# Performance work log

Measured on AMD Instinct MI355X. Metric: run time of the kernel, lower is better.

## Reference

```python
import jax, jax.numpy as jnp
import numpy as np

N_NODES = 100000
N_EDGES = 1600000
IN_CH, HID_CH, OUT_CH = 128, 128, 40


def setup_inputs() -> dict:
    key = jax.random.key(0)
    ks = jax.random.split(key, 7)
    s = 1.0 / np.sqrt(IN_CH)
    s2 = 1.0 / np.sqrt(HID_CH)
    return {
        "x": jax.random.normal(ks[0], (N_NODES, IN_CH), jnp.float32),
        "edge_index": jax.random.randint(ks[1], (2, N_EDGES), 0, N_NODES, jnp.int64),
        "W1l": jax.random.normal(ks[2], (IN_CH, HID_CH), jnp.float32) * s,
        "b1": jnp.zeros((HID_CH,), jnp.float32),
        "W1r": jax.random.normal(ks[3], (IN_CH, HID_CH), jnp.float32) * s,
        "W2l": jax.random.normal(ks[4], (HID_CH, OUT_CH), jnp.float32) * s2,
        "b2": jnp.zeros((OUT_CH,), jnp.float32),
        "W2r": jax.random.normal(ks[5], (HID_CH, OUT_CH), jnp.float32) * s2,
    }


def reference(x, edge_index, W1l, b1, W1r, W2l, b2, W2r):
    src, dst = edge_index[0], edge_index[1]
    # per-target in-degree for mean aggregation (zero-degree nodes -> 0 output)
    deg = jax.ops.segment_sum(jnp.ones((src.shape[0],), x.dtype), dst,
                              num_segments=N_NODES)
    inv_deg = jnp.where(deg > 0, 1.0 / jnp.maximum(deg, 1.0), 0.0)[:, None]

    def sage(h, Wl, b, Wr):
        # gather source features, scatter-sum to targets, normalize -> mean
        agg = jax.ops.segment_sum(h[src], dst, num_segments=N_NODES) * inv_deg
        return agg @ Wl + b + h @ Wr

    h = jax.nn.relu(sage(x, W1l, b1, W1r))
    # F.dropout(p=0.5) defaults to training=True -> active dropout
    keep = jax.random.bernoulli(jax.random.key(42), 0.5, h.shape)
    h = jnp.where(keep, h * 2.0, 0.0)
    out = sage(h, W2l, b2, W2r)
    return jax.nn.log_softmax(out, axis=1)
```

## Files before the change

kernel.cpp:

```cpp
#include <hip/hip_runtime.h>
#include <stdint.h>
#include <stddef.h>

#define N_NODES 100000
#define N_EDGES 1600000
#define IN_CH 128
#define HID_CH 128
#define OUT_CH 40

#define NB 196
#define GCAP 10240
#define TILE_EDGES 2048
#define LCAP 40

#define N_MASK_WORDS 400000
#define N_CVT4 3200000

typedef __attribute__((ext_vector_type(8))) short bf16x8;
typedef __attribute__((ext_vector_type(8))) unsigned short u16x8;
typedef __attribute__((ext_vector_type(4))) float f32x4;

__device__ __forceinline__ ushort f2bf(float f) {
    uint32_t u = __float_as_uint(f);
    uint32_t r = (u + 0x7FFFu + ((u >> 16) & 1u)) >> 16;
    return (ushort)r;
}
__device__ __forceinline__ float bf2f(ushort u) {
    return __uint_as_float(((uint32_t)u) << 16);
}

__device__ __forceinline__ uint32_t rotl32(uint32_t x, int r) {
    return (x << r) | (x >> (32 - r));
}

__device__ __forceinline__ void threefry2x32_k42(uint32_t x0, uint32_t x1,
                                                 uint32_t& o0, uint32_t& o1) {
    const uint32_t ks0 = 0u, ks1 = 42u;
    const uint32_t ks2 = 0u ^ 42u ^ 0x1BD11BDAu;
    x0 += ks0; x1 += ks1;
    x0 += x1; x1 = rotl32(x1, 13); x1 ^= x0;
    x0 += x1; x1 = rotl32(x1, 15); x1 ^= x0;
    x0 += x1; x1 = rotl32(x1, 26); x1 ^= x0;
    x0 += x1; x1 = rotl32(x1,  6); x1 ^= x0;
    x0 += ks1; x1 += ks2 + 1u;
    x0 += x1; x1 = rotl32(x1, 17); x1 ^= x0;
    x0 += x1; x1 = rotl32(x1, 29); x1 ^= x0;
    x0 += x1; x1 = rotl32(x1, 16); x1 ^= x0;
    x0 += x1; x1 = rotl32(x1, 24); x1 ^= x0;
    x0 += ks2; x1 += ks0 + 2u;
    x0 += x1; x1 = rotl32(x1, 13); x1 ^= x0;
    x0 += x1; x1 = rotl32(x1, 15); x1 ^= x0;
    x0 += x1; x1 = rotl32(x1, 26); x1 ^= x0;
    x0 += x1; x1 = rotl32(x1,  6); x1 ^= x0;
    x0 += ks0; x1 += ks1 + 3u;
    x0 += x1; x1 = rotl32(x1, 17); x1 ^= x0;
    x0 += x1; x1 = rotl32(x1, 29); x1 ^= x0;
    x0 += x1; x1 = rotl32(x1, 16); x1 ^= x0;
    x0 += x1; x1 = rotl32(x1, 24); x1 ^= x0;
    x0 += ks1; x1 += ks2 + 4u;
    x0 += x1; x1 = rotl32(x1, 13); x1 ^= x0;
    x0 += x1; x1 = rotl32(x1, 15); x1 ^= x0;
    x0 += x1; x1 = rotl32(x1, 26); x1 ^= x0;
    x0 += x1; x1 = rotl32(x1,  6); x1 ^= x0;
    x0 += ks2; x1 += ks0 + 5u;
    o0 = x0; o1 = x1;
}

__device__ __forceinline__ void load_edge(const void* ei, bool is32, int e,
                                          int& s, int& d) {
    if (is32) {
        const int* p = (const int*)ei;
        s = p[e]; d = p[N_EDGES + e];
    } else {
        const long long* p = (const long long*)ei;
        s = (int)p[e]; d = (int)p[N_EDGES + e];
    }
}

__global__ __launch_bounds__(256) void prep(const int* __restrict__ ei32,
                                            int* __restrict__ flag,
                                            int* __restrict__ gcnt) {
    const int t = threadIdx.x;
    if (blockIdx.x == 0) {
        __shared__ int red[256];
        int local = 0;
        #pragma unroll
        for (int j = 0; j < 64; ++j) {
            int k = (t * 64 + j) * 97;
            local |= ei32[2 * k + 1];
        }
        red[t] = local;
        __syncthreads();
        for (int off = 128; off; off >>= 1) {
            if (t < off) red[t] |= red[t + off];
            __syncthreads();
        }
        if (t == 0) *flag = (red[0] != 0);
    } else {
        for (int i = t; i < NB * 16; i += 256) gcnt[i] = 0;
    }
}

__global__ __launch_bounds__(256) void bucket_edges(
    const void* __restrict__ ei, const int* __restrict__ flag,
    int* __restrict__ gcnt, uint2* __restrict__ gbuf) {
    __shared__ uint2 lbuf[NB][LCAP];
    __shared__ int lcnt[NB];
    const bool is32 = (*flag != 0);
    const int t = threadIdx.x;
    for (int b = t; b < NB; b += 256) lcnt[b] = 0;
    __syncthreads();
    const int base = blockIdx.x * TILE_EDGES;
    #pragma unroll
    for (int j = 0; j < TILE_EDGES / 256; ++j) {
        int e = base + j * 256 + t;
        if (e < N_EDGES) {
            int s, d;
            load_edge(ei, is32, e, s, d);
            int b = d >> 9;
            int pos = atomicAdd(&lcnt[b], 1);
            if (pos < LCAP) {
                lbuf[b][pos] = make_uint2((uint32_t)s, (uint32_t)d);
            } else {
                int gp = atomicAdd(&gcnt[b * 16], 1);
                gbuf[(size_t)b * GCAP + gp] = make_uint2((uint32_t)s, (uint32_t)d);
            }
        }
    }
    __syncthreads();
    if (t < NB) {
        int cnt = lcnt[t];
        if (cnt > LCAP) cnt = LCAP;
        if (cnt > 0) {
            int gp = atomicAdd(&gcnt[t * 16], cnt);
            uint2* dst = gbuf + (size_t)t * GCAP + gp;
            for (int i = 0; i < cnt; ++i) dst[i] = lbuf[t][i];
        }
    }
}

__global__ void bucket_scan(const int* __restrict__ gcnt, int* __restrict__ bbase) {
    __shared__ int s[256];
    int t = threadIdx.x;
    int tot = (t < NB) ? gcnt[t * 16] : 0;
    s[t] = tot;
    __syncthreads();
    for (int off = 1; off < 256; off <<= 1) {
        int a = (t >= off) ? s[t - off] : 0;
        __syncthreads();
        s[t] += a;
        __syncthreads();
    }
    if (t < NB) bbase[t] = s[t] - tot;
}

__global__ __launch_bounds__(256) void build_csr(
    const int* __restrict__ gcnt, const uint2* __restrict__ gbuf,
    const int* __restrict__ bbase, int* __restrict__ csr, int* __restrict__ cursor) {
    __shared__ int hist[512];
    __shared__ int excl[512];
    __shared__ int cur[512];
    __shared__ int psum[256];
    const int b = blockIdx.x;
    const int t = threadIdx.x;
    hist[t] = 0; hist[t + 256] = 0;
    __syncthreads();
    const int base = bbase[b];
    const int cnt = gcnt[b * 16];
    const uint2* src = gbuf + (size_t)b * GCAP;
    for (int i = t; i < cnt; i += 256)
        atomicAdd(&hist[src[i].y & 511], 1);
    __syncthreads();
    int h0 = hist[2 * t], h1 = hist[2 * t + 1];
    psum[t] = h0 + h1;
    __syncthreads();
    int v = psum[t];
    for (int off = 1; off < 256; off <<= 1) {
        int a = (t >= off) ? psum[t - off] : 0;
        __syncthreads();
        psum[t] += a;
        __syncthreads();
    }
    int pex = psum[t] - v;
    excl[2 * t] = pex;
    excl[2 * t + 1] = pex + h0;
    cur[2 * t] = pex;
    cur[2 * t + 1] = pex + h0;
    __syncthreads();
    for (int j = t; j < 512; j += 256) {
        int node = b * 512 + j;
        if (node < N_NODES) cursor[node] = base + excl[j] + hist[j];
    }
    for (int i = t; i < cnt; i += 256) {
        uint2 p = src[i];
        int pos = atomicAdd(&cur[p.y & 511], 1);
        csr[base + pos] = (int)p.x;
    }
}

__global__ __launch_bounds__(256) void cvt_and_mask(
    const float* __restrict__ in, ushort* __restrict__ out,
    uint32_t* __restrict__ mask) {
    const long gid = (long)blockIdx.x * blockDim.x + threadIdx.x;
    const long stride = (long)gridDim.x * blockDim.x;
    for (long i = gid; i < N_CVT4; i += stride) {
        float4 v = *reinterpret_cast<const float4*>(in + i * 4);
        ushort4 r;
        r.x = f2bf(v.x); r.y = f2bf(v.y); r.z = f2bf(v.z); r.w = f2bf(v.w);
        *reinterpret_cast<ushort4*>(out + i * 4) = r;
    }
    for (long w = gid; w < N_MASK_WORDS; w += stride) {
        uint32_t m = 0;
        #pragma unroll 4
        for (int j = 0; j < 32; ++j) {
            uint32_t o0, o1;
            threefry2x32_k42(0u, (uint32_t)w * 32u + j, o0, o1);
            m |= ((o0 ^ o1) >> 31) << j;
        }
        mask[w] = m;
    }
}

__global__ void cvt_w2(const float* __restrict__ W1l, const float* __restrict__ W1r,
                       const float* __restrict__ W2l, const float* __restrict__ W2r,
                       ushort* __restrict__ Wt1, ushort* __restrict__ Wt2) {
    int blk = blockIdx.x;
    int k = threadIdx.x;
    if (blk < 128) {
        int n = blk;
        float v = (k < 128) ? W1l[(size_t)k * 128 + n] : W1r[(size_t)(k - 128) * 128 + n];
        Wt1[(size_t)n * 256 + k] = f2bf(v);
    } else {
        int n = blk - 128;
        float v = 0.0f;
        if (n < OUT_CH)
            v = (k < 128) ? W2l[(size_t)k * 40 + n] : W2r[(size_t)(k - 128) * 40 + n];
        Wt2[(size_t)n * 256 + k] = f2bf(v);
    }
}

__global__ __launch_bounds__(256) void aggregate_mean_bf(
    const ushort* __restrict__ feat, const int* __restrict__ csr,
    const int* __restrict__ cursor, ushort* __restrict__ out) {
    int node = blockIdx.x * 4 + (threadIdx.x >> 6);
    if (node >= N_NODES) return;
    const int lane = threadIdx.x & 63;
    const int g = lane >> 4;
    const int c = lane & 15;
    const int beg = (node > 0) ? cursor[node - 1] : 0;
    const int end = cursor[node];

    float acc[8];
    #pragma unroll
    for (int j = 0; j < 8; ++j) acc[j] = 0.0f;

    int e = beg + g;
    for (; e + 4 < end; e += 8) {
        int s0 = csr[e];
        int s1 = csr[e + 4];
        bf16x8 v0 = *reinterpret_cast<const bf16x8*>(feat + (size_t)s0 * 128 + c * 8);
        bf16x8 v1 = *reinterpret_cast<const bf16x8*>(feat + (size_t)s1 * 128 + c * 8);
        #pragma unroll
        for (int j = 0; j < 8; ++j) acc[j] += bf2f((ushort)v0[j]);
        #pragma unroll
        for (int j = 0; j < 8; ++j) acc[j] += bf2f((ushort)v1[j]);
    }
    if (e < end) {
        int s0 = csr[e];
        bf16x8 v0 = *reinterpret_cast<const bf16x8*>(feat + (size_t)s0 * 128 + c * 8);
        #pragma unroll
        for (int j = 0; j < 8; ++j) acc[j] += bf2f((ushort)v0[j]);
    }

    #pragma unroll
    for (int j = 0; j < 8; ++j) {
        acc[j] += __shfl_xor(acc[j], 16, 64);
        acc[j] += __shfl_xor(acc[j], 32, 64);
    }

    if (g == 0) {
        int deg = end - beg;
        float inv = (deg > 0) ? (1.0f / (float)deg) : 0.0f;
        u16x8 r;
        #pragma unroll
        for (int j = 0; j < 8; ++j) r[j] = f2bf(acc[j] * inv);
        *reinterpret_cast<u16x8*>(out + (size_t)node * 128 + c * 8) = r;
    }
}

__global__ __launch_bounds__(256) void layer1_mfma(
    const ushort* __restrict__ agg, const ushort* __restrict__ xbf,
    const ushort* __restrict__ Wt, const float* __restrict__ b1,
    const uint32_t* __restrict__ dmask, ushort* __restrict__ h) {
    const int tid = threadIdx.x;
    const int lane = tid & 63;
    const int l15 = lane & 15, kg = lane >> 4;
    const int wid = blockIdx.x * 4 + (tid >> 6);
    const int row_base = wid * 16;
    if (row_base >= N_NODES) return;
    int r0 = row_base + l15;
    int r0c = (r0 < N_NODES) ? r0 : (N_NODES - 1);

    f32x4 acc[8];
    #pragma unroll
    for (int nf = 0; nf < 8; ++nf) acc[nf] = (f32x4){0.f, 0.f, 0.f, 0.f};

    #pragma unroll
    for (int ks = 0; ks < 8; ++ks) {
        const int kglob = ks * 32 + kg * 8;
        const ushort* abase = (kglob < 128) ? agg : xbf;
        const int koff = (kglob < 128) ? kglob : (kglob - 128);
        bf16x8 a0 = *reinterpret_cast<const bf16x8*>(abase + (size_t)r0c * 128 + koff);
        #pragma unroll
        for (int nf = 0; nf < 8; ++nf) {
            bf16x8 b = *reinterpret_cast<const bf16x8*>(
                Wt + (size_t)(nf * 16 + l15) * 256 + ks * 32 + kg * 8);
            acc[nf] = __builtin_amdgcn_mfma_f32_16x16x32_bf16(a0, b, acc[nf], 0, 0, 0);
        }
    }

    #pragma unroll
    for (int r = 0; r < 4; ++r) {
        int row = row_base + kg * 4 + r;
        if (row < N_NODES) {
            uint4 mw = *reinterpret_cast<const uint4*>(dmask + (size_t)row * 4);
            const uint32_t* mwp = reinterpret_cast<const uint32_t*>(&mw);
            #pragma unroll
            for (int nf = 0; nf < 8; ++nf) {
                int col = nf * 16 + l15;
                float v = acc[nf][r] + b1[col];
                v = fmaxf(v, 0.0f) * 2.0f;
                if ((mwp[col >> 5] >> (col & 31)) & 1u) v = 0.0f;
                h[(size_t)row * 128 + col] = f2bf(v);
            }
        }
    }
}

__global__ __launch_bounds__(256) void layer2_mfma(
    const ushort* __restrict__ agg, const ushort* __restrict__ hbf,
    const ushort* __restrict__ Wt2, const float* __restrict__ b2,
    float* __restrict__ out) {
    const int tid = threadIdx.x;
    const int lane = tid & 63;
    const int l15 = lane & 15, kg = lane >> 4;
    const int wid = blockIdx.x * 4 + (tid >> 6);
    const int row_base = wid * 16;
    if (row_base >= N_NODES) return;
    int r0 = row_base + l15;
    int r0c = (r0 < N_NODES) ? r0 : (N_NODES - 1);

    f32x4 acc[3];
    #pragma unroll
    for (int nf = 0; nf < 3; ++nf) acc[nf] = (f32x4){0.f, 0.f, 0.f, 0.f};

    #pragma unroll
    for (int ks = 0; ks < 8; ++ks) {
        const int kglob = ks * 32 + kg * 8;
        const ushort* abase = (kglob < 128) ? agg : hbf;
        const int koff = (kglob < 128) ? kglob : (kglob - 128);
        bf16x8 a0 = *reinterpret_cast<const bf16x8*>(abase + (size_t)r0c * 128 + koff);
        #pragma unroll
        for (int nf = 0; nf < 3; ++nf) {
            bf16x8 b = *reinterpret_cast<const bf16x8*>(
                Wt2 + (size_t)(nf * 16 + l15) * 256 + ks * 32 + kg * 8);
            acc[nf] = __builtin_amdgcn_mfma_f32_16x16x32_bf16(a0, b, acc[nf], 0, 0, 0);
        }
    }

    #pragma unroll
    for (int r = 0; r < 4; ++r) {
        int row = row_base + kg * 4 + r;
        float v[3];
        #pragma unroll
        for (int nf = 0; nf < 3; ++nf) {
            int col = nf * 16 + l15;
            v[nf] = (col < OUT_CH) ? (acc[nf][r] + b2[col]) : -3.0e38f;
        }
        float mx = fmaxf(fmaxf(v[0], v[1]), v[2]);
        #pragma unroll
        for (int s = 1; s < 16; s <<= 1) mx = fmaxf(mx, __shfl_xor(mx, s, 64));
        float se = 0.0f;
        #pragma unroll
        for (int nf = 0; nf < 3; ++nf) {
            int col = nf * 16 + l15;
            if (col < OUT_CH) se += expf(v[nf] - mx);
        }
        #pragma unroll
        for (int s = 1; s < 16; s <<= 1) se += __shfl_xor(se, s, 64);
        float lz = mx + logf(se);
        if (row < N_NODES) {
            #pragma unroll
            for (int nf = 0; nf < 3; ++nf) {
                int col = nf * 16 + l15;
                if (col < OUT_CH)
                    out[(size_t)row * OUT_CH + col] = v[nf] - lz;
            }
        }
    }
}

extern "C" void kernel_launch(void* const* d_in, const int* in_sizes, int n_in,
                              void* d_out, int out_size, void* d_ws, size_t ws_size,
                              hipStream_t stream) {
    const float* x   = (const float*)d_in[0];
    const void*  ei  = d_in[1];
    const float* W1l = (const float*)d_in[2];
    const float* b1  = (const float*)d_in[3];
    const float* W1r = (const float*)d_in[4];
    const float* W2l = (const float*)d_in[5];
    const float* b2  = (const float*)d_in[6];
    const float* W2r = (const float*)d_in[7];
    float* out = (float*)d_out;

    char* ws = (char*)d_ws;
    int*      flag   = (int*)ws;
    int*      gcnt   = (int*)(ws + 4096);
    int*      bbase  = (int*)(ws + 106496);
    ushort*   x_bf   = (ushort*)(ws + 131072);
    ushort*   h_bf   = (ushort*)(ws + 131072 + 25600000);
    ushort*   agg_bf = (ushort*)(ws + 131072 + 51200000);
    ushort*   Wt1    = (ushort*)(ws + 131072 + 76800000);
    ushort*   Wt2    = (ushort*)(ws + 131072 + 76865536);
    uint2*    gbuf   = (uint2*)(ws + 77021184);
    uint32_t* dmask  = (uint32_t*)(ws + 93077504);

    char* ob = (char*)d_out;
    int* csr    = (int*)ob;
    int* cursor = (int*)(ob + 6400000);

    prep<<<2, 256, 0, stream>>>((const int*)ei, flag, gcnt);
    bucket_edges<<<(N_EDGES + TILE_EDGES - 1) / TILE_EDGES, 256, 0, stream>>>(
        ei, flag, gcnt, gbuf);
    bucket_scan<<<1, 256, 0, stream>>>(gcnt, bbase);
    build_csr<<<NB, 256, 0, stream>>>(gcnt, gbuf, bbase, csr, cursor);

    cvt_and_mask<<<2048, 256, 0, stream>>>(x, x_bf, dmask);
    cvt_w2<<<176, 256, 0, stream>>>(W1l, W1r, W2l, W2r, Wt1, Wt2);

    aggregate_mean_bf<<<(N_NODES + 3) / 4, 256, 0, stream>>>(x_bf, csr, cursor, agg_bf);
    layer1_mfma<<<(N_NODES + 63) / 64, 256, 0, stream>>>(agg_bf, x_bf, Wt1, b1, dmask, h_bf);
    aggregate_mean_bf<<<(N_NODES + 3) / 4, 256, 0, stream>>>(h_bf, csr, cursor, agg_bf);
    layer2_mfma<<<(N_NODES + 63) / 64, 256, 0, stream>>>(agg_bf, h_bf, Wt2, b2, out);
}
```

Measured before the change: 323.1 us.

## Stage weights in LDS and split layer-1 GEMM columns across blocks

Both dense-layer kernels now copy their transposed weight tile into padded shared memory once per block, and the MFMA loop reads B fragments from LDS instead of global memory. The A fragments are preloaded into registers up front. Layer 1 is split into two column halves per row tile, which doubles the grid and lowers per-thread accumulator registers. The cost is that the A rows are read twice in layer 1, and every block pays for a weight copy plus a barrier.

```diff
diff --git a/kernel.cpp b/kernel.cpp
--- a/kernel.cpp
+++ b/kernel.cpp
@@ -15,6 +15,8 @@
 
 #define N_MASK_WORDS 400000
 #define N_CVT4 3200000
+
+#define WROW 264
 
 typedef __attribute__((ext_vector_type(8))) short bf16x8;
 typedef __attribute__((ext_vector_type(8))) unsigned short u16x8;
@@ -292,30 +294,44 @@
     const ushort* __restrict__ agg, const ushort* __restrict__ xbf,
     const ushort* __restrict__ Wt, const float* __restrict__ b1,
     const uint32_t* __restrict__ dmask, ushort* __restrict__ h) {
+    __shared__ ushort wlds[64 * WROW];
     const int tid = threadIdx.x;
     const int lane = tid & 63;
     const int l15 = lane & 15, kg = lane >> 4;
-    const int wid = blockIdx.x * 4 + (tid >> 6);
-    const int row_base = wid * 16;
+    const int colBase = (blockIdx.x & 1) * 64;
+    const int row_base = ((blockIdx.x >> 1) * 4 + (tid >> 6)) * 16;
+
+    #pragma unroll
+    for (int i = 0; i < 8; ++i) {
+        int idx = tid + i * 256;
+        int r = idx >> 5, c = idx & 31;
+        u16x8 v = *reinterpret_cast<const u16x8*>(Wt + (size_t)(colBase + r) * 256 + c * 8);
+        *reinterpret_cast<u16x8*>(wlds + r * WROW + c * 8) = v;
+    }
+    __syncthreads();
     if (row_base >= N_NODES) return;
+
     int r0 = row_base + l15;
     int r0c = (r0 < N_NODES) ? r0 : (N_NODES - 1);
 
-    f32x4 acc[8];
-    #pragma unroll
-    for (int nf = 0; nf < 8; ++nf) acc[nf] = (f32x4){0.f, 0.f, 0.f, 0.f};
-
-    #pragma unroll
-    for (int ks = 0; ks < 8; ++ks) {
-        const int kglob = ks * 32 + kg * 8;
-        const ushort* abase = (kglob < 128) ? agg : xbf;
-        const int koff = (kglob < 128) ? kglob : (kglob - 128);
-        bf16x8 a0 = *reinterpret_cast<const bf16x8*>(abase + (size_t)r0c * 128 + koff);
-        #pragma unroll
-        for (int nf = 0; nf < 8; ++nf) {
-            bf16x8 b = *reinterpret_cast<const bf16x8*>(
-                Wt + (size_t)(nf * 16 + l15) * 256 + ks * 32 + kg * 8);
-            acc[nf] = __builtin_amdgcn_mfma_f32_16x16x32_bf16(a0, b, acc[nf], 0, 0, 0);
+    bf16x8 a[8];
+    #pragma unroll
+    for (int ks = 0; ks < 4; ++ks) {
+        a[ks]     = *reinterpret_cast<const bf16x8*>(agg + (size_t)r0c * 128 + ks * 32 + kg * 8);
+        a[ks + 4] = *reinterpret_cast<const bf16x8*>(xbf + (size_t)r0c * 128 + ks * 32 + kg * 8);
+    }
+
+    f32x4 acc[4];
+    #pragma unroll
+    for (int nf = 0; nf < 4; ++nf) acc[nf] = (f32x4){0.f, 0.f, 0.f, 0.f};
+
+    #pragma unroll
+    for (int nf = 0; nf < 4; ++nf) {
+        const ushort* bp = wlds + (nf * 16 + l15) * WROW + kg * 8;
+        #pragma unroll
+        for (int ks = 0; ks < 8; ++ks) {
+            bf16x8 b = *reinterpret_cast<const bf16x8*>(bp + ks * 32);
+            acc[nf] = __builtin_amdgcn_mfma_f32_16x16x32_bf16(a[ks], b, acc[nf], 0, 0, 0);
         }
     }
 
@@ -326,8 +342,8 @@
             uint4 mw = *reinterpret_cast<const uint4*>(dmask + (size_t)row * 4);
             const uint32_t* mwp = reinterpret_cast<const uint32_t*>(&mw);
             #pragma unroll
-            for (int nf = 0; nf < 8; ++nf) {
-                int col = nf * 16 + l15;
+            for (int nf = 0; nf < 4; ++nf) {
+                int col = colBase + nf * 16 + l15;
                 float v = acc[nf][r] + b1[col];
                 v = fmaxf(v, 0.0f) * 2.0f;
                 if ((mwp[col >> 5] >> (col & 31)) & 1u) v = 0.0f;
@@ -341,30 +357,43 @@
     const ushort* __restrict__ agg, const ushort* __restrict__ hbf,
     const ushort* __restrict__ Wt2, const float* __restrict__ b2,
     float* __restrict__ out) {
+    __shared__ ushort wlds[48 * WROW];
     const int tid = threadIdx.x;
     const int lane = tid & 63;
     const int l15 = lane & 15, kg = lane >> 4;
-    const int wid = blockIdx.x * 4 + (tid >> 6);
-    const int row_base = wid * 16;
+    const int row_base = (blockIdx.x * 4 + (tid >> 6)) * 16;
+
+    #pragma unroll
+    for (int i = 0; i < 6; ++i) {
+        int idx = tid + i * 256;
+        int r = idx >> 5, c = idx & 31;
+        u16x8 v = *reinterpret_cast<const u16x8*>(Wt2 + (size_t)r * 256 + c * 8);
+        *reinterpret_cast<u16x8*>(wlds + r * WROW + c * 8) = v;
+    }
+    __syncthreads();
     if (row_base >= N_NODES) return;
+
     int r0 = row_base + l15;
     int r0c = (r0 < N_NODES) ? r0 : (N_NODES - 1);
 
+    bf16x8 a[8];
+    #pragma unroll
+    for (int ks = 0; ks < 4; ++ks) {
+        a[ks]     = *reinterpret_cast<const bf16x8*>(agg + (size_t)r0c * 128 + ks * 32 + kg * 8);
+        a[ks + 4] = *reinterpret_cast<const bf16x8*>(hbf + (size_t)r0c * 128 + ks * 32 + kg * 8);
+    }
+
     f32x4 acc[3];
     #pragma unroll
     for (int nf = 0; nf < 3; ++nf) acc[nf] = (f32x4){0.f, 0.f, 0.f, 0.f};
 
     #pragma unroll
-    for (int ks = 0; ks < 8; ++ks) {
-        const int kglob = ks * 32 + kg * 8;
-        const ushort* abase = (kglob < 128) ? agg : hbf;
-        const int koff = (kglob < 128) ? kglob : (kglob - 128);
-        bf16x8 a0 = *reinterpret_cast<const bf16x8*>(abase + (size_t)r0c * 128 + koff);
-        #pragma unroll
-        for (int nf = 0; nf < 3; ++nf) {
-            bf16x8 b = *reinterpret_cast<const bf16x8*>(
-                Wt2 + (size_t)(nf * 16 + l15) * 256 + ks * 32 + kg * 8);
-            acc[nf] = __builtin_amdgcn_mfma_f32_16x16x32_bf16(a0, b, acc[nf], 0, 0, 0);
+    for (int nf = 0; nf < 3; ++nf) {
+        const ushort* bp = wlds + (nf * 16 + l15) * WROW + kg * 8;
+        #pragma unroll
+        for (int ks = 0; ks < 8; ++ks) {
+            bf16x8 b = *reinterpret_cast<const bf16x8*>(bp + ks * 32);
+            acc[nf] = __builtin_amdgcn_mfma_f32_16x16x32_bf16(a[ks], b, acc[nf], 0, 0, 0);
         }
     }
 
@@ -439,7 +468,7 @@
     cvt_w2<<<176, 256, 0, stream>>>(W1l, W1r, W2l, W2r, Wt1, Wt2);
 
     aggregate_mean_bf<<<(N_NODES + 3) / 4, 256, 0, stream>>>(x_bf, csr, cursor, agg_bf);
-    layer1_mfma<<<(N_NODES + 63) / 64, 256, 0, stream>>>(agg_bf, x_bf, Wt1, b1, dmask, h_bf);
+    layer1_mfma<<<2 * ((N_NODES + 63) / 64), 256, 0, stream>>>(agg_bf, x_bf, Wt1, b1, dmask, h_bf);
     aggregate_mean_bf<<<(N_NODES + 3) / 4, 256, 0, stream>>>(h_bf, csr, cursor, agg_bf);
     layer2_mfma<<<(N_NODES + 63) / 64, 256, 0, stream>>>(agg_bf, h_bf, Wt2, b2, out);
 }
```

Measured after the change: 293.7 us. 1.1x faster.
